# Kernel optimization log

Hardware: AMD Instinct MI355X
Metric: run time of the kernel (lower is better)

## Reference

```python
import jax, jax.numpy as jnp
import numpy as np

VOCAB = 32000
EMBED = 512
HIDDEN = 1024
MAX_VOCAB = 33000
MAX_LEN = 128
BATCH = 64


def setup_inputs() -> dict:
    key = jax.random.key(0)
    ks = jax.random.split(key, 20)
    s = 0.02
    H, E, L, V = HIDDEN, EMBED, MAX_LEN, VOCAB
    return {
        "input_tok": jax.random.randint(ks[0], (BATCH,), 0, V, dtype=jnp.int64 if jax.config.jax_enable_x64 else jnp.int32),
        "hidden": jax.random.normal(ks[1], (1, BATCH, H), jnp.float32),
        "encoder_outputs": jax.random.normal(ks[2], (BATCH, L, H), jnp.float32),
        "input_seq": jax.random.randint(ks[3], (BATCH, L), 0, V, dtype=jnp.int64 if jax.config.jax_enable_x64 else jnp.int32),
        "pre_prob": jax.random.uniform(ks[4], (BATCH, L), jnp.float32),
        "emb": jax.random.normal(ks[5], (V, E), jnp.float32) * s,
        "attn_W": jax.random.normal(ks[6], (L, H + E), jnp.float32) * s,
        "attn_b": jnp.zeros((L,), jnp.float32),
        "comb_W": jax.random.normal(ks[7], (H, H + E), jnp.float32) * s,
        "comb_b": jnp.zeros((H,), jnp.float32),
        "W_ih": jax.random.normal(ks[8], (3 * H, 2 * H), jnp.float32) * s,
        "W_hh": jax.random.normal(ks[9], (3 * H, H), jnp.float32) * s,
        "b_ih": jnp.zeros((3 * H,), jnp.float32),
        "b_hh": jnp.zeros((3 * H,), jnp.float32),
        "Wo_W": jax.random.normal(ks[10], (V, H), jnp.float32) * s,
        "Wo_b": jnp.zeros((V,), jnp.float32),
        "Wc_W": jax.random.normal(ks[11], (H, H), jnp.float32) * s,
        "Wc_b": jnp.zeros((H,), jnp.float32),
    }


def _decoder_step(input_tok, hidden, encoder_outputs, input_seq, pre_prob,
                  emb, attn_W, attn_b, comb_W, comb_b,
                  W_ih, W_hh, b_ih, b_hh, Wo_W, Wo_b, Wc_W, Wc_b):
    B = encoder_outputs.shape[0]
    H = hidden.shape[-1]
    V = Wo_W.shape[0]
    # selective read: mask where previous output token matches source tokens
    sel = (input_tok[:, None] == input_seq).astype(pre_prob.dtype) * pre_prob  # [B,L]
    # torch does encoder_outputs.long().float() -> truncation toward zero
    sel_reading = jnp.einsum('bl,blh->bh', sel, jnp.trunc(encoder_outputs))  # [B,H]

    embedded = emb[input_tok]  # [B,E] (dropout is identity in eval)
    h = hidden[0]  # [B,H]

    a = jnp.concatenate([embedded, h], axis=1) @ attn_W.T + attn_b  # [B,L]
    attn_weights = jax.nn.softmax(a, axis=1)
    attn_applied = jnp.einsum('bl,blh->bh', attn_weights, encoder_outputs)  # [B,H]

    out = jnp.concatenate([embedded, attn_applied], axis=1) @ comb_W.T + comb_b
    out = jax.nn.relu(out)  # [B,H]

    gru_in = jnp.concatenate([out, sel_reading], axis=1)  # [B,2H]
    gi = gru_in @ W_ih.T + b_ih  # [B,3H]
    gh = h @ W_hh.T + b_hh       # [B,3H]
    i_r, i_z, i_n = jnp.split(gi, 3, axis=1)
    h_r, h_z, h_n = jnp.split(gh, 3, axis=1)
    r = jax.nn.sigmoid(i_r + h_r)
    z = jax.nn.sigmoid(i_z + h_z)
    n = jnp.tanh(i_n + r * h_n)
    h_new = (1.0 - z) * n + z * h  # [B,H]

    score_g = h_new @ Wo_W.T + Wo_b  # [B,V]
    score_c = jnp.tanh(encoder_outputs @ Wc_W.T + Wc_b)  # [B,L,H]
    score_c = jnp.einsum('blh,bh->bl', score_c, h_new)   # [B,L]

    score = jax.nn.softmax(jnp.concatenate([score_g, score_c], axis=1), axis=1)
    prob_g = score[:, :V]
    prob_c = score[:, V:]  # [B,L]

    output1 = jnp.concatenate(
        [prob_g, jnp.zeros((B, MAX_VOCAB - V), prob_g.dtype)], axis=1)  # [B,MAX_VOCAB]
    # bmm(prob_c, one_hot(input_seq)) == scatter-add of copy probs onto vocab ids
    b_idx = jnp.arange(B)[:, None]
    output1 = output1.at[b_idx, input_seq].add(prob_c)
    output1 = jnp.where(output1 == 0, 1e-9, output1)
    output1 = output1.at[:, 2].set(1e-9)
    output1 = jnp.log(output1)
    return output1, h_new[None], attn_weights, prob_c


def reference(input_tok, hidden, encoder_outputs, input_seq, pre_prob,
              emb, attn_W, attn_b, comb_W, comb_b,
              W_ih, W_hh, b_ih, b_hh, Wo_W, Wo_b, Wc_W, Wc_b):
    return _decoder_step(input_tok, hidden, encoder_outputs, input_seq, pre_prob,
                         emb, attn_W, attn_b, comb_W, comb_b,
                         W_ih, W_hh, b_ih, b_hh, Wo_W, Wo_b, Wc_W, Wc_b)
```

## Files before the change

kernel.cpp:

```cpp
#include <hip/hip_runtime.h>
#include <math.h>

#define BB 64
#define LL 128
#define HH 1024
#define EE 512
#define VV 32000
#define MAXV 33000

typedef float f32x4 __attribute__((ext_vector_type(4)));
typedef short bf16x8 __attribute__((ext_vector_type(8)));
typedef unsigned u32x4 __attribute__((ext_vector_type(4)));

__device__ __forceinline__ void gload_lds16(const void* g, void* l) {
    __builtin_amdgcn_global_load_lds((const __attribute__((address_space(1))) void*)g,
                                     (__attribute__((address_space(3))) void*)l, 16, 0, 0);
}

__device__ __forceinline__ unsigned short f2bf(float f) {
    unsigned u = __float_as_uint(f);
    return (unsigned short)((u + 0x7fffu + ((u >> 16) & 1u)) >> 16);
}

__device__ __forceinline__ unsigned pkbf(float a, float b) {
    unsigned r;
    asm("v_cvt_pk_bf16_f32 %0, %1, %2" : "=v"(r) : "v"(a), "v"(b));
    return r;
}

__device__ __forceinline__ void smerge(float& m, float& s, float m2, float s2) {
    float nm = fmaxf(m, m2);
    s = s * expf(m - nm) + s2 * expf(m2 - nm);
    m = nm;
}

__device__ __forceinline__ float ftanh(float x) {
    return 1.f - 2.f / (1.f + __expf(2.f * x));
}

__global__ void cvt_bf16(const float* __restrict__ in, unsigned short* __restrict__ out, int n4) {
    int i = blockIdx.x * 256 + threadIdx.x;
    if (i >= n4) return;
    float4 v = ((const float4*)in)[i];
    ushort4 o;
    o.x = f2bf(v.x); o.y = f2bf(v.y); o.z = f2bf(v.z); o.w = f2bf(v.w);
    ((ushort4*)out)[i] = o;
}

__global__ void setup(const float* __restrict__ WcW, unsigned short* __restrict__ WcB,
                      const int* __restrict__ tok, const float* __restrict__ hidden,
                      const float* __restrict__ emb, unsigned short* __restrict__ xaB,
                      const float* __restrict__ attnb, const float* __restrict__ combb,
                      const float* __restrict__ bih, const float* __restrict__ bhh,
                      float* __restrict__ aT, float* __restrict__ gruOutF,
                      float* __restrict__ giT, float* __restrict__ ghT,
                      float* __restrict__ zeros, float* __restrict__ out1) {
    int idx = blockIdx.x * 256 + threadIdx.x;
    if (idx < 262144) {
        float4 v = ((const float4*)WcW)[idx];
        ushort4 o;
        o.x = f2bf(v.x); o.y = f2bf(v.y); o.z = f2bf(v.z); o.w = f2bf(v.w);
        ((ushort4*)WcB)[idx] = o;
        return;
    }
    idx -= 262144;
    if (idx < 98304) {
        int b = idx / 1536, k = idx % 1536;
        float v = (k < EE) ? emb[tok[b] * EE + k] : hidden[b * HH + (k - EE)];
        xaB[b * 1536 + k] = f2bf(v);
        return;
    }
    idx -= 98304;
    if (idx < 8192) { aT[idx] = attnb[idx >> 6]; return; }
    idx -= 8192;
    if (idx < 65536) { gruOutF[idx] = combb[idx >> 6]; return; }
    idx -= 65536;
    if (idx < 196608) { giT[idx] = bih[idx >> 6]; return; }
    idx -= 196608;
    if (idx < 196608) { ghT[idx] = bhh[idx >> 6]; return; }
    idx -= 196608;
    if (idx < 139264) { zeros[idx] = 0.f; return; }
    idx -= 139264;
    int b = idx / 8000, q = idx % 8000;
    ((float4*)(out1 + (size_t)b * MAXV))[q] = (float4){0.f, 0.f, 0.f, 0.f};
}

template <int DIRECT, int MI>
__device__ __forceinline__ void mgemm_body(int bid,
        const float* __restrict__ W, const float* __restrict__ bias,
        const unsigned short* __restrict__ xA, int sA,
        const unsigned short* __restrict__ xB, int sB, int K1,
        int K, int Kc, int splitk, float* __restrict__ out) {
    int tid = threadIdx.x, w = tid >> 6, lane = tid & 63;
    int rb = bid / splitk, kseg = bid - rb * splitk;
    int r0 = rb * (MI * 64), kb0 = kseg * Kc;
    int lr = lane & 15, lk = lane >> 4;
    int nt = Kc >> 6;
    f32x4 acc[MI][4];
#pragma unroll
    for (int mi = 0; mi < MI; ++mi)
#pragma unroll
        for (int nf = 0; nf < 4; ++nf) acc[mi][nf] = (f32x4){0.f, 0.f, 0.f, 0.f};
    const float* Wr[MI];
#pragma unroll
    for (int mi = 0; mi < MI; ++mi)
        Wr[mi] = W + (size_t)(r0 + w * (MI * 16) + mi * 16 + lr) * K;

    for (int t = 0; t < nt; ++t) {
        int kb = kb0 + t * 64;
        bf16x8 bfr[2][4];
#pragma unroll
        for (int ks = 0; ks < 2; ++ks)
#pragma unroll
            for (int nf = 0; nf < 4; ++nf) {
                int bcol = nf * 16 + lr;
                int kg = kb + ks * 32 + lk * 8;
                const unsigned short* xp = (kg < K1) ? (xA + bcol * sA + kg)
                                                     : (xB + bcol * sB + (kg - K1));
                bfr[ks][nf] = *(const bf16x8*)xp;
            }
        bf16x8 afr[MI][2];
#pragma unroll
        for (int mi = 0; mi < MI; ++mi)
#pragma unroll
            for (int ks = 0; ks < 2; ++ks) {
                const float* wp = Wr[mi] + kb + ks * 32 + lk * 8;
                float4 w0 = *(const float4*)wp;
                float4 w1 = *(const float4*)(wp + 4);
                union { u32x4 u; bf16x8 h; } cv;
                cv.u[0] = pkbf(w0.x, w0.y); cv.u[1] = pkbf(w0.z, w0.w);
                cv.u[2] = pkbf(w1.x, w1.y); cv.u[3] = pkbf(w1.z, w1.w);
                afr[mi][ks] = cv.h;
            }
#pragma unroll
        for (int ks = 0; ks < 2; ++ks)
#pragma unroll
            for (int mi = 0; mi < MI; ++mi)
#pragma unroll
                for (int nf = 0; nf < 4; ++nf)
                    acc[mi][nf] = __builtin_amdgcn_mfma_f32_16x16x32_bf16(
                        afr[mi][ks], bfr[ks][nf], acc[mi][nf], 0, 0, 0);
    }
#pragma unroll
    for (int mi = 0; mi < MI; ++mi)
#pragma unroll
        for (int nf = 0; nf < 4; ++nf)
#pragma unroll
            for (int reg = 0; reg < 4; ++reg) {
                int r = r0 + w * (MI * 16) + mi * 16 + lk * 4 + reg;
                int bcol = nf * 16 + lr;
                float v = acc[mi][nf][reg];
                if (DIRECT) out[r * 64 + bcol] = v + bias[r];
                else atomicAdd(&out[r * 64 + bcol], v);
            }
}

template <int DIRECT, int MI>
__global__ __launch_bounds__(256) void mgemm(
        const float* __restrict__ W, const float* __restrict__ bias,
        const unsigned short* __restrict__ xA, int sA,
        const unsigned short* __restrict__ xB, int sB, int K1,
        int K, int Kc, int splitk, float* __restrict__ out) {
    mgemm_body<DIRECT, MI>(blockIdx.x, W, bias, xA, sA, xB, sB, K1, K, Kc, splitk, out);
}

__global__ __launch_bounds__(256) void gru2(
        const float* __restrict__ Wih, const float* __restrict__ Whh,
        const unsigned short* __restrict__ gruInB, const unsigned short* __restrict__ xaB512,
        float* __restrict__ giT, float* __restrict__ ghT) {
    const float* W; const unsigned short* x; int s, K1, K, Kc; float* out; int bid;
    if (blockIdx.x < 96) { W = Wih; x = gruInB; s = 2048; K1 = 2048; K = 2048; Kc = 512; out = giT; bid = blockIdx.x; }
    else                 { W = Whh; x = xaB512; s = 1536; K1 = 1024; K = 1024; Kc = 256; out = ghT; bid = blockIdx.x - 96; }
    mgemm_body<0, 2>(bid, W, nullptr, x, s, x, s, K1, K, Kc, 4, out);
}

__global__ __launch_bounds__(256) void k2_softmax_enc(
        const float* __restrict__ aT, const int* __restrict__ tok, const int* __restrict__ seq,
        const float* __restrict__ pprob, const float* __restrict__ enc,
        float* __restrict__ ap4T, float* __restrict__ gruSelF, float* __restrict__ out3) {
    int b = blockIdx.x, lc = blockIdx.y, t = threadIdx.x;
    __shared__ float red[256];
    __shared__ float w_s[32], sel_s[32];
    float av = (t < LL) ? aT[t * 64 + b] : -1e30f;
    red[t] = av; __syncthreads();
    for (int s = 128; s > 0; s >>= 1) { if (t < s) red[t] = fmaxf(red[t], red[t + s]); __syncthreads(); }
    float m = red[0]; __syncthreads();
    float e = (t < LL) ? expf(av - m) : 0.f;
    red[t] = e; __syncthreads();
    for (int s = 128; s > 0; s >>= 1) { if (t < s) red[t] += red[t + s]; __syncthreads(); }
    float Z = red[0]; __syncthreads();
    if (t < LL) {
        float wv = e / Z;
        if (lc == 0) out3[b * LL + t] = wv;
        int l0 = lc * 32;
        if (t >= l0 && t < l0 + 32) {
            w_s[t - l0] = wv;
            sel_s[t - l0] = (seq[b * LL + t] == tok[b]) ? pprob[b * LL + t] : 0.f;
        }
    }
    __syncthreads();
    float accA[4] = {0.f,0.f,0.f,0.f}, accS[4] = {0.f,0.f,0.f,0.f};
    const float* encb = enc + (size_t)b * LL * HH + (size_t)lc * 32 * HH;
    for (int l = 0; l < 32; ++l) {
        float wl = w_s[l], sl = sel_s[l];
#pragma unroll
        for (int i = 0; i < 4; ++i) {
            float ev = encb[l * HH + t + i * 256];
            accA[i] += wl * ev;
            accS[i] += sl * truncf(ev);
        }
    }
#pragma unroll
    for (int i = 0; i < 4; ++i) {
        int h = t + i * 256;
        atomicAdd(&ap4T[(h >> 2) * 256 + b * 4 + (h & 3)], accA[i]);
        atomicAdd(&gruSelF[(h >> 2) * 256 + b * 4 + (h & 3)], accS[i]);
    }
}

__global__ void cvt_ap(const float* __restrict__ ap4T, unsigned short* __restrict__ apB) {
    int tid = blockIdx.x * 256 + threadIdx.x;
    int b = tid & 63, kq = tid >> 6;
    float4 v = *(const float4*)&ap4T[kq * 256 + b * 4];
    ushort4 o;
    o.x = f2bf(v.x); o.y = f2bf(v.y); o.z = f2bf(v.z); o.w = f2bf(v.w);
    *(ushort4*)&apB[b * 1024 + kq * 4] = o;
}

__global__ void cvt_gruIn(const float* __restrict__ gruOutF, const float* __restrict__ gruSelF,
                          unsigned short* __restrict__ gruInB) {
    int tid = blockIdx.x * 256 + threadIdx.x;
    int b = tid & 63, kq = tid >> 6;
    float4 v;
    if (kq < 256) {
        int k = kq * 4;
        v.x = fmaxf(gruOutF[(k + 0) * 64 + b], 0.f);
        v.y = fmaxf(gruOutF[(k + 1) * 64 + b], 0.f);
        v.z = fmaxf(gruOutF[(k + 2) * 64 + b], 0.f);
        v.w = fmaxf(gruOutF[(k + 3) * 64 + b], 0.f);
    } else {
        v = *(const float4*)&gruSelF[(kq - 256) * 256 + b * 4];
    }
    ushort4 o;
    o.x = f2bf(v.x); o.y = f2bf(v.y); o.z = f2bf(v.z); o.w = f2bf(v.w);
    *(ushort4*)&gruInB[b * 2048 + kq * 4] = o;
}

__global__ void k5_gates(const float* __restrict__ giT, const float* __restrict__ ghT,
                         const float* __restrict__ hidden, float* __restrict__ hn4T,
                         unsigned short* __restrict__ hnB, float* __restrict__ out2) {
    int idx = blockIdx.x * 256 + threadIdx.x;
    int r = idx >> 6, b = idx & 63;
    float ir = giT[r * 64 + b], iz = giT[(HH + r) * 64 + b], in_ = giT[(2 * HH + r) * 64 + b];
    float hr = ghT[r * 64 + b], hz = ghT[(HH + r) * 64 + b], hn = ghT[(2 * HH + r) * 64 + b];
    float rr = 1.f / (1.f + expf(-(ir + hr)));
    float zz = 1.f / (1.f + expf(-(iz + hz)));
    float nn = tanhf(in_ + rr * hn);
    float hprev = hidden[b * HH + r];
    float hnew = (1.f - zz) * nn + zz * hprev;
    hn4T[(r >> 2) * 256 + b * 4 + (r & 3)] = hnew;
    hnB[b * 1024 + r] = f2bf(hnew);
    out2[b * HH + r] = hnew;
}

__global__ __launch_bounds__(256) void wow_f1(
        const float* __restrict__ WoW, const float* __restrict__ Wob,
        const unsigned short* __restrict__ hnB, float* __restrict__ sgT,
        float* __restrict__ partMt, float* __restrict__ partSt) {
    __shared__ float pm_s[4 * 64], ps_s[4 * 64];
    int tid = threadIdx.x, w = tid >> 6, lane = tid & 63;
    int lr = lane & 15, lk = lane >> 4;
    int r0 = blockIdx.x * 64;
    f32x4 acc[4];
#pragma unroll
    for (int nf = 0; nf < 4; ++nf) acc[nf] = (f32x4){0.f, 0.f, 0.f, 0.f};
    const float* Wr = WoW + (size_t)(r0 + w * 16 + lr) * HH;
    for (int t = 0; t < 16; ++t) {
        int kb = t * 64;
        bf16x8 bfr[2][4];
#pragma unroll
        for (int ks = 0; ks < 2; ++ks)
#pragma unroll
            for (int nf = 0; nf < 4; ++nf)
                bfr[ks][nf] = *(const bf16x8*)(hnB + (nf * 16 + lr) * 1024 + kb + ks * 32 + lk * 8);
        bf16x8 afr[2];
#pragma unroll
        for (int ks = 0; ks < 2; ++ks) {
            const float* wp = Wr + kb + ks * 32 + lk * 8;
            float4 w0 = *(const float4*)wp;
            float4 w1 = *(const float4*)(wp + 4);
            union { u32x4 u; bf16x8 h; } cv;
            cv.u[0] = pkbf(w0.x, w0.y); cv.u[1] = pkbf(w0.z, w0.w);
            cv.u[2] = pkbf(w1.x, w1.y); cv.u[3] = pkbf(w1.z, w1.w);
            afr[ks] = cv.h;
        }
#pragma unroll
        for (int ks = 0; ks < 2; ++ks)
#pragma unroll
            for (int nf = 0; nf < 4; ++nf)
                acc[nf] = __builtin_amdgcn_mfma_f32_16x16x32_bf16(afr[ks], bfr[ks][nf], acc[nf], 0, 0, 0);
    }
#pragma unroll
    for (int nf = 0; nf < 4; ++nf) {
        int bcol = nf * 16 + lr;
        float m = -1e30f, s = 0.f;
#pragma unroll
        for (int reg = 0; reg < 4; ++reg) {
            int r = r0 + w * 16 + lk * 4 + reg;
            float v = acc[nf][reg] + Wob[r];
            sgT[r * 64 + bcol] = v;
            float nm = fmaxf(m, v);
            s = s * expf(m - nm) + expf(v - nm);
            m = nm;
        }
#pragma unroll
        for (int d = 16; d <= 32; d <<= 1) {
            float om = __shfl_xor(m, d), os = __shfl_xor(s, d);
            smerge(m, s, om, os);
        }
        if (lk == 0) { pm_s[w * 64 + bcol] = m; ps_s[w * 64 + bcol] = s; }
    }
    __syncthreads();
    if (tid < 64) {
        float m = pm_s[tid], s = ps_s[tid];
        smerge(m, s, pm_s[64 + tid], ps_s[64 + tid]);
        smerge(m, s, pm_s[128 + tid], ps_s[128 + tid]);
        smerge(m, s, pm_s[192 + tid], ps_s[192 + tid]);
        partMt[tid * 512 + blockIdx.x] = m;
        partSt[tid * 512 + blockIdx.x] = s;
    }
}

__global__ __launch_bounds__(256) void k7_mfma(const unsigned short* __restrict__ encB,
        const unsigned short* __restrict__ WcB, const float* __restrict__ Wcb,
        const float* __restrict__ hn4T, float* __restrict__ sc) {
    __shared__ __align__(16) unsigned short As[128 * 64];
    __shared__ __align__(16) unsigned short Bs[128 * 64];
    __shared__ float h_s[128], bias_s[128];
    int tid = threadIdx.x, w = tid >> 6, lane = tid & 63;
    int wm = w >> 1, wn = w & 1;
    int bid = blockIdx.x;
    int swz = (bid & 7) * 64 + (bid >> 3);
    int mt = swz >> 3, nt = swz & 7;
    int m0 = mt * 128, n0 = nt * 128;
    if (tid < 128) {
        int n = n0 + tid;
        bias_s[tid] = Wcb[n];
        h_s[tid] = hn4T[(n >> 2) * 256 + mt * 4 + (n & 3)];
    }
    f32x4 acc[4][4];
#pragma unroll
    for (int mi = 0; mi < 4; ++mi)
#pragma unroll
        for (int ni = 0; ni < 4; ++ni) acc[mi][ni] = (f32x4){0.f, 0.f, 0.f, 0.f};

    for (int kt = 0; kt < 16; ++kt) {
        __syncthreads();
#pragma unroll
        for (int i = 0; i < 4; ++i) {
            int c = i * 256 + tid;
            int row = c >> 3, cc = c & 7;
            int lc2 = cc ^ (row & 7);
            gload_lds16(encB + (size_t)(m0 + row) * HH + kt * 64 + lc2 * 8,
                        (char*)As + (i * 256 + w * 64) * 16);
        }
#pragma unroll
        for (int i = 0; i < 4; ++i) {
            int c = i * 256 + tid;
            int row = c >> 3, cc = c & 7;
            int lc2 = cc ^ (row & 7);
            gload_lds16(WcB + (size_t)(n0 + row) * HH + kt * 64 + lc2 * 8,
                        (char*)Bs + (i * 256 + w * 64) * 16);
        }
        asm volatile("s_waitcnt vmcnt(0)");
        __syncthreads();
#pragma unroll
        for (int ks = 0; ks < 2; ++ks) {
            bf16x8 af[4], bf[4];
#pragma unroll
            for (int mi = 0; mi < 4; ++mi) {
                int rr = wm * 64 + mi * 16 + (lane & 15);
                int lkk = ks * 4 + (lane >> 4);
                af[mi] = *(const bf16x8*)((const char*)As + rr * 128 + ((lkk ^ (rr & 7)) * 16));
            }
#pragma unroll
            for (int ni = 0; ni < 4; ++ni) {
                int rr = wn * 64 + ni * 16 + (lane & 15);
                int lkk = ks * 4 + (lane >> 4);
                bf[ni] = *(const bf16x8*)((const char*)Bs + rr * 128 + ((lkk ^ (rr & 7)) * 16));
            }
#pragma unroll
            for (int mi = 0; mi < 4; ++mi)
#pragma unroll
                for (int ni = 0; ni < 4; ++ni)
                    acc[mi][ni] = __builtin_amdgcn_mfma_f32_16x16x32_bf16(af[mi], bf[ni], acc[mi][ni], 0, 0, 0);
        }
    }
    float rs[16];
#pragma unroll
    for (int z = 0; z < 16; ++z) rs[z] = 0.f;
#pragma unroll
    for (int ni = 0; ni < 4; ++ni) {
        int nl = wn * 64 + ni * 16 + (lane & 15);
        float hv = h_s[nl], bv = bias_s[nl];
#pragma unroll
        for (int mi = 0; mi < 4; ++mi)
#pragma unroll
            for (int reg = 0; reg < 4; ++reg)
                rs[mi * 4 + reg] += ftanh(acc[mi][ni][reg] + bv) * hv;
    }
#pragma unroll
    for (int z = 0; z < 16; ++z) {
        float v = rs[z];
        v += __shfl_xor(v, 1); v += __shfl_xor(v, 2);
        v += __shfl_xor(v, 4); v += __shfl_xor(v, 8);
        rs[z] = v;
    }
    if ((lane & 15) == 0) {
        int g = lane >> 4;
#pragma unroll
        for (int mi = 0; mi < 4; ++mi)
#pragma unroll
            for (int reg = 0; reg < 4; ++reg)
                atomicAdd(&sc[mt * LL + wm * 64 + mi * 16 + g * 4 + reg], rs[mi * 4 + reg]);
    }
}

__global__ __launch_bounds__(256) void f1c_final(const float* __restrict__ partMt,
        const float* __restrict__ partSt, const float* __restrict__ sc,
        const int* __restrict__ seq, float* __restrict__ Mb, float* __restrict__ Zb,
        float* __restrict__ out4, float* __restrict__ out1) {
    int b = blockIdx.x, t = threadIdx.x;
    __shared__ float mred[256], sred[256];
    float m = -1e30f, s = 0.f;
    for (int w = t; w < 500; w += 256)
        smerge(m, s, partMt[b * 512 + w], partSt[b * 512 + w]);
    if (t < 128) smerge(m, s, sc[b * LL + t], 1.0f);
    mred[t] = m; sred[t] = s; __syncthreads();
    for (int st = 128; st > 0; st >>= 1) {
        if (t < st) {
            float mm = mred[t], ss = sred[t];
            smerge(mm, ss, mred[t + st], sred[t + st]);
            mred[t] = mm; sred[t] = ss;
        }
        __syncthreads();
    }
    float M = mred[0], Z = sred[0];
    if (t == 0) { Mb[b] = M; Zb[b] = Z; }
    if (t < 128) {
        float p = expf(sc[b * LL + t] - M) / Z;
        out4[b * LL + t] = p;
        atomicAdd(&out1[(size_t)b * MAXV + seq[b * LL + t]], p);
    }
}

__global__ void f2f4_final(const float* __restrict__ sgT, const float* __restrict__ Mb,
                           const float* __restrict__ Zb, float* __restrict__ out1) {
    int b = blockIdx.y;
    int v = blockIdx.x * 256 + threadIdx.x;
    if (v >= MAXV) return;
    float val = 0.f;
    if (v < VV) {
        float scat = out1[(size_t)b * MAXV + v];
        val = expf(sgT[v * 64 + b] - Mb[b]) / Zb[b] + scat;
    }
    if (v == 2 || val == 0.f) val = 1e-9f;
    out1[(size_t)b * MAXV + v] = logf(val);
}

extern "C" void kernel_launch(void* const* d_in, const int* in_sizes, int n_in,
                              void* d_out, int out_size, void* d_ws, size_t ws_size,
                              hipStream_t stream) {
    (void)in_sizes; (void)n_in; (void)out_size; (void)ws_size;
    const int*   tok    = (const int*)  d_in[0];
    const float* hidden = (const float*)d_in[1];
    const float* enc    = (const float*)d_in[2];
    const int*   seq    = (const int*)  d_in[3];
    const float* pprob  = (const float*)d_in[4];
    const float* emb    = (const float*)d_in[5];
    const float* attnW  = (const float*)d_in[6];
    const float* attnb  = (const float*)d_in[7];
    const float* combW  = (const float*)d_in[8];
    const float* combb  = (const float*)d_in[9];
    const float* Wih    = (const float*)d_in[10];
    const float* Whh    = (const float*)d_in[11];
    const float* bih    = (const float*)d_in[12];
    const float* bhh    = (const float*)d_in[13];
    const float* WoW    = (const float*)d_in[14];
    const float* Wob    = (const float*)d_in[15];
    const float* WcW    = (const float*)d_in[16];
    const float* Wcb    = (const float*)d_in[17];

    float* out1 = (float*)d_out;
    float* out2 = out1 + (size_t)BB * MAXV;
    float* out3 = out2 + BB * HH;
    float* out4 = out3 + BB * LL;

    float* ws      = (float*)d_ws;
    float* aT      = ws;
    float* ap4T    = ws + 8192;
    float* gruSelF = ws + 73728;
    float* sc      = ws + 139264;
    float* gruOutF = ws + 147456;
    float* giT     = ws + 212992;
    float* ghT     = ws + 409600;
    float* hn4T    = ws + 606208;
    float* sgT     = ws + 671744;
    float* partMt  = ws + 2719744;
    float* partSt  = ws + 2752512;
    float* Mb      = ws + 2785280;
    float* Zb      = ws + 2785344;
    unsigned short* encB = (unsigned short*)(ws + 2785408);
    unsigned short* WcB  = encB + 8388608;
    unsigned short* hnB  = (unsigned short*)(ws + 7504000);
    unsigned short* xaB    = (unsigned short*)sgT;
    unsigned short* apB    = (unsigned short*)(ws + 720896);
    unsigned short* gruInB = (unsigned short*)(ws + 753664);

    cvt_bf16     <<<8192, 256, 0, stream>>>(enc, encB, 2097152);
    setup        <<<5776, 256, 0, stream>>>(WcW, WcB, tok, hidden, emb, xaB,
                                            attnb, combb, bih, bhh,
                                            aT, gruOutF, giT, ghT, ap4T, out1);
    mgemm<0,2>   <<<6, 256, 0, stream>>>(attnW, nullptr, xaB, 1536, xaB, 1536, 1536, 1536, 256, 6, aT);
    k2_softmax_enc<<<dim3(64, 4), 256, 0, stream>>>(aT, tok, seq, pprob, enc, ap4T, gruSelF, out3);
    cvt_ap       <<<64, 256, 0, stream>>>(ap4T, apB);
    mgemm<0,2>   <<<24, 256, 0, stream>>>(combW, nullptr, xaB, 1536, apB, 1024, 512, 1536, 512, 3, gruOutF);
    cvt_gruIn    <<<128, 256, 0, stream>>>(gruOutF, gruSelF, gruInB);
    gru2         <<<192, 256, 0, stream>>>(Wih, Whh, gruInB, xaB + 512, giT, ghT);
    k5_gates     <<<256, 256, 0, stream>>>(giT, ghT, hidden, hn4T, hnB, out2);
    wow_f1       <<<500, 256, 0, stream>>>(WoW, Wob, hnB, sgT, partMt, partSt);
    k7_mfma      <<<512, 256, 0, stream>>>(encB, WcB, Wcb, hn4T, sc);
    f1c_final    <<<64, 256, 0, stream>>>(partMt, partSt, sc, seq, Mb, Zb, out4, out1);
    f2f4_final   <<<dim3(129, 64), 256, 0, stream>>>(sgT, Mb, Zb, out1);
}
```

Before: 194.3 us.

## Merge enc conversion into setup, raise split-K parallelism, use fast exp/log

Folds the encoder fp32-to-bf16 conversion into the setup kernel, removing one launch. Doubles or quadruples the split-K factor and block counts for the attention, combine and GRU GEMMs, and halves the L-chunk per block in the attention-softmax/encoder kernel, so more CUs are busy on these small GEMMs. Replaces expf/logf/tanhf with __expf/__logf and a fast tanh. The cost is more atomic traffic from the larger split-K, plus slightly lower precision in the transcendentals.

```diff
diff --git a/kernel.cpp b/kernel.cpp
--- a/kernel.cpp
+++ b/kernel.cpp
@@ -28,34 +28,35 @@
     return r;
 }
 
+__device__ __forceinline__ float fexp(float x) { return __expf(x); }
+__device__ __forceinline__ float flog(float x) { return __logf(x); }
+__device__ __forceinline__ float ftanh(float x) { return 1.f - 2.f / (1.f + __expf(2.f * x)); }
+
 __device__ __forceinline__ void smerge(float& m, float& s, float m2, float s2) {
     float nm = fmaxf(m, m2);
-    s = s * expf(m - nm) + s2 * expf(m2 - nm);
+    s = s * fexp(m - nm) + s2 * fexp(m2 - nm);
     m = nm;
 }
 
-__device__ __forceinline__ float ftanh(float x) {
-    return 1.f - 2.f / (1.f + __expf(2.f * x));
-}
-
-__global__ void cvt_bf16(const float* __restrict__ in, unsigned short* __restrict__ out, int n4) {
-    int i = blockIdx.x * 256 + threadIdx.x;
-    if (i >= n4) return;
-    float4 v = ((const float4*)in)[i];
-    ushort4 o;
-    o.x = f2bf(v.x); o.y = f2bf(v.y); o.z = f2bf(v.z); o.w = f2bf(v.w);
-    ((ushort4*)out)[i] = o;
-}
-
-__global__ void setup(const float* __restrict__ WcW, unsigned short* __restrict__ WcB,
-                      const int* __restrict__ tok, const float* __restrict__ hidden,
-                      const float* __restrict__ emb, unsigned short* __restrict__ xaB,
-                      const float* __restrict__ attnb, const float* __restrict__ combb,
-                      const float* __restrict__ bih, const float* __restrict__ bhh,
-                      float* __restrict__ aT, float* __restrict__ gruOutF,
-                      float* __restrict__ giT, float* __restrict__ ghT,
-                      float* __restrict__ zeros, float* __restrict__ out1) {
+#define N_ENC4 2097152
+__global__ void setup2(const float* __restrict__ enc, unsigned short* __restrict__ encB,
+                       const float* __restrict__ WcW, unsigned short* __restrict__ WcB,
+                       const int* __restrict__ tok, const float* __restrict__ hidden,
+                       const float* __restrict__ emb, unsigned short* __restrict__ xaB,
+                       const float* __restrict__ attnb, const float* __restrict__ combb,
+                       const float* __restrict__ bih, const float* __restrict__ bhh,
+                       float* __restrict__ aT, float* __restrict__ gruOutF,
+                       float* __restrict__ giT, float* __restrict__ ghT,
+                       float* __restrict__ zeros, float* __restrict__ out1) {
     int idx = blockIdx.x * 256 + threadIdx.x;
+    if (idx < N_ENC4) {
+        float4 v = ((const float4*)enc)[idx];
+        ushort4 o;
+        o.x = f2bf(v.x); o.y = f2bf(v.y); o.z = f2bf(v.z); o.w = f2bf(v.w);
+        ((ushort4*)encB)[idx] = o;
+        return;
+    }
+    idx -= N_ENC4;
     if (idx < 262144) {
         float4 v = ((const float4*)WcW)[idx];
         ushort4 o;
@@ -169,9 +170,9 @@
         const unsigned short* __restrict__ gruInB, const unsigned short* __restrict__ xaB512,
         float* __restrict__ giT, float* __restrict__ ghT) {
     const float* W; const unsigned short* x; int s, K1, K, Kc; float* out; int bid;
-    if (blockIdx.x < 96) { W = Wih; x = gruInB; s = 2048; K1 = 2048; K = 2048; Kc = 512; out = giT; bid = blockIdx.x; }
-    else                 { W = Whh; x = xaB512; s = 1536; K1 = 1024; K = 1024; Kc = 256; out = ghT; bid = blockIdx.x - 96; }
-    mgemm_body<0, 2>(bid, W, nullptr, x, s, x, s, K1, K, Kc, 4, out);
+    if (blockIdx.x < 192) { W = Wih; x = gruInB; s = 2048; K1 = 2048; K = 2048; Kc = 256; out = giT; bid = blockIdx.x; }
+    else                  { W = Whh; x = xaB512; s = 1536; K1 = 1024; K = 1024; Kc = 128; out = ghT; bid = blockIdx.x - 192; }
+    mgemm_body<0, 2>(bid, W, nullptr, x, s, x, s, K1, K, Kc, 8, out);
 }
 
 __global__ __launch_bounds__(256) void k2_softmax_enc(
@@ -180,28 +181,28 @@
         float* __restrict__ ap4T, float* __restrict__ gruSelF, float* __restrict__ out3) {
     int b = blockIdx.x, lc = blockIdx.y, t = threadIdx.x;
     __shared__ float red[256];
-    __shared__ float w_s[32], sel_s[32];
+    __shared__ float w_s[16], sel_s[16];
     float av = (t < LL) ? aT[t * 64 + b] : -1e30f;
     red[t] = av; __syncthreads();
     for (int s = 128; s > 0; s >>= 1) { if (t < s) red[t] = fmaxf(red[t], red[t + s]); __syncthreads(); }
     float m = red[0]; __syncthreads();
-    float e = (t < LL) ? expf(av - m) : 0.f;
+    float e = (t < LL) ? fexp(av - m) : 0.f;
     red[t] = e; __syncthreads();
     for (int s = 128; s > 0; s >>= 1) { if (t < s) red[t] += red[t + s]; __syncthreads(); }
     float Z = red[0]; __syncthreads();
     if (t < LL) {
         float wv = e / Z;
         if (lc == 0) out3[b * LL + t] = wv;
-        int l0 = lc * 32;
-        if (t >= l0 && t < l0 + 32) {
+        int l0 = lc * 16;
+        if (t >= l0 && t < l0 + 16) {
             w_s[t - l0] = wv;
             sel_s[t - l0] = (seq[b * LL + t] == tok[b]) ? pprob[b * LL + t] : 0.f;
         }
     }
     __syncthreads();
     float accA[4] = {0.f,0.f,0.f,0.f}, accS[4] = {0.f,0.f,0.f,0.f};
-    const float* encb = enc + (size_t)b * LL * HH + (size_t)lc * 32 * HH;
-    for (int l = 0; l < 32; ++l) {
+    const float* encb = enc + (size_t)b * LL * HH + (size_t)lc * 16 * HH;
+    for (int l = 0; l < 16; ++l) {
         float wl = w_s[l], sl = sel_s[l];
 #pragma unroll
         for (int i = 0; i < 4; ++i) {
@@ -253,9 +254,9 @@
     int r = idx >> 6, b = idx & 63;
     float ir = giT[r * 64 + b], iz = giT[(HH + r) * 64 + b], in_ = giT[(2 * HH + r) * 64 + b];
     float hr = ghT[r * 64 + b], hz = ghT[(HH + r) * 64 + b], hn = ghT[(2 * HH + r) * 64 + b];
-    float rr = 1.f / (1.f + expf(-(ir + hr)));
-    float zz = 1.f / (1.f + expf(-(iz + hz)));
-    float nn = tanhf(in_ + rr * hn);
+    float rr = 1.f / (1.f + fexp(-(ir + hr)));
+    float zz = 1.f / (1.f + fexp(-(iz + hz)));
+    float nn = ftanh(in_ + rr * hn);
     float hprev = hidden[b * HH + r];
     float hnew = (1.f - zz) * nn + zz * hprev;
     hn4T[(r >> 2) * 256 + b * 4 + (r & 3)] = hnew;
@@ -310,7 +311,7 @@
             float v = acc[nf][reg] + Wob[r];
             sgT[r * 64 + bcol] = v;
             float nm = fmaxf(m, v);
-            s = s * expf(m - nm) + expf(v - nm);
+            s = s * fexp(m - nm) + fexp(v - nm);
             m = nm;
         }
 #pragma unroll
@@ -448,7 +449,7 @@
     float M = mred[0], Z = sred[0];
     if (t == 0) { Mb[b] = M; Zb[b] = Z; }
     if (t < 128) {
-        float p = expf(sc[b * LL + t] - M) / Z;
+        float p = fexp(sc[b * LL + t] - M) / Z;
         out4[b * LL + t] = p;
         atomicAdd(&out1[(size_t)b * MAXV + seq[b * LL + t]], p);
     }
@@ -462,10 +463,10 @@
     float val = 0.f;
     if (v < VV) {
         float scat = out1[(size_t)b * MAXV + v];
-        val = expf(sgT[v * 64 + b] - Mb[b]) / Zb[b] + scat;
+        val = fexp(sgT[v * 64 + b] - Mb[b]) / Zb[b] + scat;
     }
     if (v == 2 || val == 0.f) val = 1e-9f;
-    out1[(size_t)b * MAXV + v] = logf(val);
+    out1[(size_t)b * MAXV + v] = flog(val);
 }
 
 extern "C" void kernel_launch(void* const* d_in, const int* in_sizes, int n_in,
@@ -517,16 +518,15 @@
     unsigned short* apB    = (unsigned short*)(ws + 720896);
     unsigned short* gruInB = (unsigned short*)(ws + 753664);
 
-    cvt_bf16     <<<8192, 256, 0, stream>>>(enc, encB, 2097152);
-    setup        <<<5776, 256, 0, stream>>>(WcW, WcB, tok, hidden, emb, xaB,
-                                            attnb, combb, bih, bhh,
-                                            aT, gruOutF, giT, ghT, ap4T, out1);
-    mgemm<0,2>   <<<6, 256, 0, stream>>>(attnW, nullptr, xaB, 1536, xaB, 1536, 1536, 1536, 256, 6, aT);
-    k2_softmax_enc<<<dim3(64, 4), 256, 0, stream>>>(aT, tok, seq, pprob, enc, ap4T, gruSelF, out3);
+    setup2       <<<13968, 256, 0, stream>>>(enc, encB, WcW, WcB, tok, hidden, emb, xaB,
+                                             attnb, combb, bih, bhh,
+                                             aT, gruOutF, giT, ghT, ap4T, out1);
+    mgemm<0,2>   <<<12, 256, 0, stream>>>(attnW, nullptr, xaB, 1536, xaB, 1536, 1536, 1536, 128, 12, aT);
+    k2_softmax_enc<<<dim3(64, 8), 256, 0, stream>>>(aT, tok, seq, pprob, enc, ap4T, gruSelF, out3);
     cvt_ap       <<<64, 256, 0, stream>>>(ap4T, apB);
-    mgemm<0,2>   <<<24, 256, 0, stream>>>(combW, nullptr, xaB, 1536, apB, 1024, 512, 1536, 512, 3, gruOutF);
+    mgemm<0,2>   <<<96, 256, 0, stream>>>(combW, nullptr, xaB, 1536, apB, 1024, 512, 1536, 128, 12, gruOutF);
     cvt_gruIn    <<<128, 256, 0, stream>>>(gruOutF, gruSelF, gruInB);
-    gru2         <<<192, 256, 0, stream>>>(Wih, Whh, gruInB, xaB + 512, giT, ghT);
+    gru2         <<<384, 256, 0, stream>>>(Wih, Whh, gruInB, xaB + 512, giT, ghT);
     k5_gates     <<<256, 256, 0, stream>>>(giT, ghT, hidden, hn4T, hnB, out2);
     wow_f1       <<<500, 256, 0, stream>>>(WoW, Wob, hnB, sgT, partMt, partSt);
     k7_mfma      <<<512, 256, 0, stream>>>(encB, WcB, Wcb, hn4T, sc);
```

New measurement: 174.4 us. 1.11x faster.
